# Kernel tuning notes

Measured on AMD Instinct MI355X. Metric: run time of the kernel, lower is better.

Reference implementation:

```python
import jax, jax.numpy as jnp
import numpy as np

E = 1024
H = 16
DH = E // H
FF = 4 * E
EPS = 1e-5


def _layer_norm(x, g, b):
    mu = jnp.mean(x, axis=-1, keepdims=True)
    var = jnp.var(x, axis=-1, keepdims=True)
    return (x - mu) * jax.lax.rsqrt(var + EPS) * g + b


def setup_inputs() -> dict:
    key = jax.random.key(0)
    ks = jax.random.split(key, 12)
    B, S = 2, 2048
    s_e = 1.0 / np.sqrt(E)
    s_f = 1.0 / np.sqrt(FF)
    return {
        "hidden_states": jax.random.normal(ks[0], (B, S, E), jnp.float32),
        "attention_mask": jnp.zeros((B, S), jnp.float32),
        "position_bias": jax.random.normal(ks[1], (H, S, S), jnp.float32) * 0.1,
        "Wq": jax.random.normal(ks[2], (E, E), jnp.float32) * s_e,
        "bq": jnp.zeros((E,), jnp.float32),
        "Wk": jax.random.normal(ks[3], (E, E), jnp.float32) * s_e,
        "bk": jnp.zeros((E,), jnp.float32),
        "Wv": jax.random.normal(ks[4], (E, E), jnp.float32) * s_e,
        "bv": jnp.zeros((E,), jnp.float32),
        "Wo": jax.random.normal(ks[5], (E, E), jnp.float32) * s_e,
        "bo": jnp.zeros((E,), jnp.float32),
        "ln1_g": jnp.ones((E,), jnp.float32),
        "ln1_b": jnp.zeros((E,), jnp.float32),
        "W1": jax.random.normal(ks[6], (E, FF), jnp.float32) * s_e,
        "b1": jnp.zeros((FF,), jnp.float32),
        "W2": jax.random.normal(ks[7], (FF, E), jnp.float32) * s_f,
        "b2": jnp.zeros((E,), jnp.float32),
        "ln2_g": jnp.ones((E,), jnp.float32),
        "ln2_b": jnp.zeros((E,), jnp.float32),
    }


def reference(hidden_states, attention_mask, position_bias, Wq, bq, Wk, bk, Wv, bv,
              Wo, bo, ln1_g, ln1_b, W1, b1, W2, b2, ln2_g, ln2_b):
    B, S, _ = hidden_states.shape
    x = hidden_states
    # QKV projections, split heads: [B, S, H, DH]
    q = (x @ Wq + bq).reshape(B, S, H, DH)
    k = (x @ Wk + bk).reshape(B, S, H, DH)
    v = (x @ Wv + bv).reshape(B, S, H, DH)
    # scores: [B, H, S, S]
    scores = jnp.einsum("bshd,bthd->bhst", q, k) / np.sqrt(DH).astype(np.float32)
    scores = scores + position_bias[None] + attention_mask[:, None, None, :]
    probs = jax.nn.softmax(scores, axis=-1)  # dropout is identity in eval
    ctx = jnp.einsum("bhst,bthd->bshd", probs, v).reshape(B, S, E)
    attn_out = ctx @ Wo + bo
    h = _layer_norm(x + attn_out, ln1_g, ln1_b)
    ffn = jax.nn.gelu(h @ W1 + b1, approximate=False) @ W2 + b2
    return _layer_norm(h + ffn, ln2_g, ln2_b)
```

## Files before the change

### kernel.cpp

```cpp
#include <hip/hip_runtime.h>
#include <stdint.h>

#define EDIM   1024
#define NHEAD  16
#define DHEAD  64
#define FFDIM  4096
#define SEQLEN 2048
#define NBATCH 2
#define MROWS  (NBATCH * SEQLEN)
#define NT     (SEQLEN / 64)

typedef __attribute__((ext_vector_type(8))) short bf16x8;
typedef __attribute__((ext_vector_type(4))) float f32x4;

static __device__ __forceinline__ unsigned short f2bf(float f) {
    union { float f; uint32_t u; } v; v.f = f;
    return (unsigned short)((v.u + 0x7fffu + ((v.u >> 16) & 1u)) >> 16);
}

static __device__ __forceinline__ void gload16(const void* g, void* s) {
    __builtin_amdgcn_global_load_lds(
        (const __attribute__((address_space(1))) unsigned int*)g,
        (__attribute__((address_space(3))) unsigned int*)s,
        16, 0, 0);
}

static __device__ __forceinline__ float gelu_f(float x) {
    float z = 0.7978845608028654f * (x + 0.044715f * x * x * x);
    float e = __expf(-2.0f * fabsf(z));
    float th = (1.0f - e) / (1.0f + e);
    th = (z >= 0.0f) ? th : -th;
    return 0.5f * x * (1.0f + th);
}

__global__ void k_cast_bf16(const float* __restrict__ in, unsigned short* __restrict__ out, int n4) {
    int i = blockIdx.x * blockDim.x + threadIdx.x;
    if (i < n4) {
        float4 v = ((const float4*)in)[i];
        ushort4 o;
        o.x = f2bf(v.x); o.y = f2bf(v.y); o.z = f2bf(v.z); o.w = f2bf(v.w);
        ((ushort4*)out)[i] = o;
    }
}

__global__ void k_transpose_cast(const float* __restrict__ in, unsigned short* __restrict__ out,
                                 int R, int C) {
    __shared__ float tile[32][33];
    int c0 = blockIdx.x * 32, r0 = blockIdx.y * 32;
    int tx = threadIdx.x, ty = threadIdx.y;
    #pragma unroll
    for (int i = 0; i < 32; i += 8)
        tile[ty + i][tx] = in[(size_t)(r0 + ty + i) * C + c0 + tx];
    __syncthreads();
    #pragma unroll
    for (int i = 0; i < 32; i += 8)
        out[(size_t)(c0 + ty + i) * R + r0 + tx] = f2bf(tile[tx][ty + i]);
}

__global__ void k_transpose_cast4(const float* __restrict__ s0, const float* __restrict__ s1,
                                  const float* __restrict__ s2, const float* __restrict__ s3,
                                  unsigned short* __restrict__ d0, unsigned short* __restrict__ d1,
                                  unsigned short* __restrict__ d2, unsigned short* __restrict__ d3) {
    __shared__ float tile[32][33];
    const int z = blockIdx.z;
    const float* in = (z == 0) ? s0 : (z == 1) ? s1 : (z == 2) ? s2 : s3;
    unsigned short* out = (z == 0) ? d0 : (z == 1) ? d1 : (z == 2) ? d2 : d3;
    int c0 = blockIdx.x * 32, r0 = blockIdx.y * 32;
    int tx = threadIdx.x, ty = threadIdx.y;
    #pragma unroll
    for (int i = 0; i < 32; i += 8)
        tile[ty + i][tx] = in[(size_t)(r0 + ty + i) * EDIM + c0 + tx];
    __syncthreads();
    #pragma unroll
    for (int i = 0; i < 32; i += 8)
        out[(size_t)(c0 + ty + i) * EDIM + r0 + tx] = f2bf(tile[tx][ty + i]);
}

__global__ void k_transpose_v(const unsigned short* __restrict__ V, int vstride,
                              unsigned short* __restrict__ Vt) {
    __shared__ unsigned short tile[32][33];
    const int bh = blockIdx.z, b = bh >> 4, h = bh & 15;
    const int s0 = blockIdx.x * 32, d0 = blockIdx.y * 32;
    const int tx = threadIdx.x, ty = threadIdx.y;
    #pragma unroll
    for (int i = 0; i < 32; i += 8)
        tile[ty + i][tx] = V[(size_t)(b * SEQLEN + s0 + ty + i) * vstride + h * DHEAD + d0 + tx];
    __syncthreads();
    #pragma unroll
    for (int i = 0; i < 32; i += 8)
        Vt[((size_t)(b * NHEAD + h) * DHEAD + d0 + ty + i) * SEQLEN + s0 + tx] = tile[tx][ty + i];
}

__global__ void k_concat_bias(const float* __restrict__ bq, const float* __restrict__ bk,
                              const float* __restrict__ bv, float* __restrict__ out) {
    int i = blockIdx.x * 256 + threadIdx.x;
    const float* src = (i < 1024) ? bq : (i < 2048) ? bk : bv;
    out[i] = src[i & 1023];
}

template <int TBM, int TBN, int EPI, int SPLITK>
__global__ __launch_bounds__(256, 3) void k_gemm(
    const unsigned short* __restrict__ A,
    const unsigned short* __restrict__ Bt,
    const float* __restrict__ bias,
    void* __restrict__ Cout, int M, int N, int K)
{
    constexpr int MR = TBM / 32, NR = TBN / 32;
    __shared__ __attribute__((aligned(16))) unsigned short Asm[TBM * 64];
    __shared__ __attribute__((aligned(16))) unsigned short Bsm[TBN * 64];

    const int nbx = gridDim.x;
    const int flat = blockIdx.y * nbx + blockIdx.x;
    const int cpx = (nbx * gridDim.y) >> 3;
    const int swz = (flat & 7) * cpx + (flat >> 3);
    const int bx = swz % nbx, by = swz / nbx;
    const int kz = (SPLITK > 1) ? blockIdx.z : 0;
    const int Ksub = K / SPLITK;

    const int row0 = by * TBM, col0 = bx * TBN;
    const int t = threadIdx.x;
    const int lane = t & 63, w = t >> 6;
    const int wm = w >> 1, wn = w & 1;
    const int l15 = lane & 15, l4 = lane >> 4;
    const int sr = lane >> 3, sc = (lane & 7) * 8;

    f32x4 acc[MR][NR];
    #pragma unroll
    for (int m = 0; m < MR; ++m)
        #pragma unroll
        for (int n = 0; n < NR; ++n) acc[m][n] = (f32x4){0.f, 0.f, 0.f, 0.f};

    for (int k0 = kz * Ksub; k0 < (kz + 1) * Ksub; k0 += 64) {
        #pragma unroll
        for (int i = 0; i < TBM / 32; ++i) {
            const int r = w * (TBM / 4) + i * 8;
            gload16(A + (size_t)(row0 + r + sr) * K + k0 + sc, &Asm[r * 64]);
        }
        #pragma unroll
        for (int i = 0; i < TBN / 32; ++i) {
            const int r = w * (TBN / 4) + i * 8;
            gload16(Bt + (size_t)(col0 + r + sr) * K + k0 + sc, &Bsm[r * 64]);
        }
        __syncthreads();
        #pragma unroll
        for (int kk = 0; kk < 64; kk += 32) {
            bf16x8 af[MR], bf[NR];
            #pragma unroll
            for (int m = 0; m < MR; ++m)
                af[m] = *(const bf16x8*)&Asm[(wm * (TBM / 2) + m * 16 + l15) * 64 + kk + l4 * 8];
            #pragma unroll
            for (int n = 0; n < NR; ++n)
                bf[n] = *(const bf16x8*)&Bsm[(wn * (TBN / 2) + n * 16 + l15) * 64 + kk + l4 * 8];
            #pragma unroll
            for (int m = 0; m < MR; ++m)
                #pragma unroll
                for (int n = 0; n < NR; ++n)
                    acc[m][n] = __builtin_amdgcn_mfma_f32_16x16x32_bf16(af[m], bf[n], acc[m][n], 0, 0, 0);
        }
        __syncthreads();
    }

    #pragma unroll
    for (int m = 0; m < MR; ++m) {
        int rb = row0 + wm * (TBM / 2) + m * 16 + l4 * 4;
        #pragma unroll
        for (int n = 0; n < NR; ++n) {
            int c = col0 + wn * (TBN / 2) + n * 16 + l15;
            float bv = (SPLITK == 1 || kz == 0) ? bias[c] : 0.0f;
            #pragma unroll
            for (int i = 0; i < 4; ++i) {
                float v = acc[m][n][i] + bv;
                if (EPI == 1) v = gelu_f(v);
                if (EPI == 2) {
                    float* outp = (float*)Cout + (size_t)kz * M * N;
                    outp[(size_t)(rb + i) * N + c] = v;
                } else {
                    ((unsigned short*)Cout)[(size_t)(rb + i) * N + c] = f2bf(v);
                }
            }
        }
    }
}

__global__ __launch_bounds__(512, 2) void k_attn(
    const unsigned short* __restrict__ QKV,
    const unsigned short* __restrict__ Vt,
    const float* __restrict__ pbias,
    const float* __restrict__ mask,
    unsigned short* __restrict__ Ctx)
{
    __shared__ __attribute__((aligned(16))) unsigned short Ksm[2][2][64 * 64];
    __shared__ __attribute__((aligned(16))) unsigned short Vsm[2][2][64 * 64];
    __shared__ __attribute__((aligned(16))) unsigned short Psm[8][16 * 32];

    const int flat = blockIdx.x;
    const int swz = (flat & 7) * 64 + (flat >> 3);
    const int qt = swz & 31;
    const int h  = swz >> 5;

    const int t = threadIdx.x;
    const int lane = t & 63, w = t >> 6;
    const int wb = w & 1;
    const int wq = (w >> 1) * 16;
    const int l15 = lane & 15, l4 = lane >> 4;
    const int qrow = qt * 64 + wq;

    const float* pbrow = pbias + ((size_t)h * SEQLEN + qrow + l4 * 4) * SEQLEN;
    const float* mrow  = mask + wb * SEQLEN;

    bf16x8 qf0, qf1;
    {
        const unsigned short* qp = QKV + (size_t)(wb * SEQLEN + qrow + l15) * (3 * EDIM) + h * DHEAD + l4 * 8;
        bf16x8 r0 = *(const bf16x8*)qp;
        bf16x8 r1 = *(const bf16x8*)(qp + 32);
        #pragma unroll
        for (int e = 0; e < 8; ++e) {
            union { uint32_t u; float f; } c0, c1;
            c0.u = (uint32_t)(unsigned short)r0[e] << 16;
            c1.u = (uint32_t)(unsigned short)r1[e] << 16;
            r0[e] = (short)f2bf(c0.f * 0.125f);
            r1[e] = (short)f2bf(c1.f * 0.125f);
        }
        qf0 = r0; qf1 = r1;
    }

    f32x4 oacc[4];
    #pragma unroll
    for (int nd = 0; nd < 4; ++nd) oacc[nd] = (f32x4){0.f, 0.f, 0.f, 0.f};
    float m_run[4] = {-1e30f, -1e30f, -1e30f, -1e30f};
    float l_run[4] = {0.f, 0.f, 0.f, 0.f};

    const int srow = lane >> 3;
    const int schk = lane & 7;
    const int r7 = l15 & 7;

    auto stage = [&](int buf, int kt) {
        const int kbase = kt * 64;
        #pragma unroll
        for (int j = 0; j < 4; ++j) {
            const int q  = w * 4 + j;
            const int kv = q >> 4;
            const int bb = (q >> 3) & 1;
            const int g  = q & 7;
            const int row = g * 8 + srow;
            const int cg  = (schk ^ (row & 7)) * 8;
            if (kv == 0)
                gload16(QKV + (size_t)(bb * SEQLEN + kbase + row) * (3 * EDIM) + EDIM + h * DHEAD + cg,
                        &Ksm[buf][bb][g * 512]);
            else
                gload16(Vt + ((size_t)((bb * NHEAD + h) * DHEAD) + row) * SEQLEN + kbase + cg,
                        &Vsm[buf][bb][g * 512]);
        }
    };

    auto compute = [&](int buf, int kt) {
        const int kbase = kt * 64;
        float p[4][4];
        float tmax[4] = {-1e30f, -1e30f, -1e30f, -1e30f};
        #pragma unroll
        for (int n = 0; n < 4; ++n) {
            const int scol = kbase + n * 16 + l15;
            const float mk = mrow[scol];
            f32x4 z;
            #pragma unroll
            for (int i = 0; i < 4; ++i) z[i] = pbrow[(size_t)i * SEQLEN + scol] + mk;
            bf16x8 kb0 = *(const bf16x8*)&Ksm[buf][wb][(n * 16 + l15) * 64 + ((l4 ^ r7) << 3)];
            bf16x8 kb1 = *(const bf16x8*)&Ksm[buf][wb][(n * 16 + l15) * 64 + (((4 + l4) ^ r7) << 3)];
            z = __builtin_amdgcn_mfma_f32_16x16x32_bf16(qf0, kb0, z, 0, 0, 0);
            z = __builtin_amdgcn_mfma_f32_16x16x32_bf16(qf1, kb1, z, 0, 0, 0);
            #pragma unroll
            for (int i = 0; i < 4; ++i) {
                p[n][i] = z[i];
                tmax[i] = fmaxf(tmax[i], z[i]);
            }
        }
        #pragma unroll
        for (int i = 0; i < 4; ++i) {
            float mv = tmax[i];
            #pragma unroll
            for (int off = 1; off < 16; off <<= 1) mv = fmaxf(mv, __shfl_xor(mv, off, 64));
            float mnew = fmaxf(m_run[i], mv);
            float alpha = __expf(m_run[i] - mnew);
            m_run[i] = mnew;
            float sum = 0.f;
            #pragma unroll
            for (int n = 0; n < 4; ++n) { p[n][i] = __expf(p[n][i] - mnew); sum += p[n][i]; }
            #pragma unroll
            for (int off = 1; off < 16; off <<= 1) sum += __shfl_xor(sum, off, 64);
            l_run[i] = l_run[i] * alpha + sum;
            #pragma unroll
            for (int nd = 0; nd < 4; ++nd) oacc[nd][i] *= alpha;
        }
        #pragma unroll
        for (int hh = 0; hh < 2; ++hh) {
            #pragma unroll
            for (int n = 0; n < 2; ++n)
                #pragma unroll
                for (int i = 0; i < 4; ++i) {
                    const int row = l4 * 4 + i;
                    const int cl = n * 16 + l15;
                    Psm[w][row * 32 + (((cl >> 3) ^ (row & 3)) << 3) + (cl & 7)] =
                        f2bf(p[2 * hh + n][i]);
                }
            bf16x8 pa = *(const bf16x8*)&Psm[w][l15 * 32 + ((l4 ^ (l15 & 3)) << 3)];
            #pragma unroll
            for (int nd = 0; nd < 4; ++nd) {
                bf16x8 vf = *(const bf16x8*)&Vsm[buf][wb][(nd * 16 + l15) * 64 + (((hh * 4 + l4) ^ r7) << 3)];
                oacc[nd] = __builtin_amdgcn_mfma_f32_16x16x32_bf16(pa, vf, oacc[nd], 0, 0, 0);
            }
        }
    };

    stage(0, 0);
    __syncthreads();
    int buf = 0;
    for (int kt = 0; kt < NT; ++kt) {
        stage(buf ^ 1, (kt + 1) & (NT - 1));
        compute(buf, kt);
        __syncthreads();
        buf ^= 1;
    }

    #pragma unroll
    for (int nd = 0; nd < 4; ++nd)
        #pragma unroll
        for (int i = 0; i < 4; ++i) {
            float v = oacc[nd][i] / l_run[i];
            Ctx[(size_t)(wb * SEQLEN + qrow + l4 * 4 + i) * EDIM + h * DHEAD + nd * 16 + l15] = f2bf(v);
        }
}

template <int WRITE_BF>
__global__ __launch_bounds__(256) void k_ln(
    const float* __restrict__ X, const float* __restrict__ T, const float* __restrict__ T2,
    const float* __restrict__ gam, const float* __restrict__ bet,
    float* __restrict__ Of, unsigned short* __restrict__ Ob)
{
    const int r = blockIdx.x;
    const int t = threadIdx.x;
    const size_t base = (size_t)r * EDIM + t * 4;
    float4 xv = *(const float4*)(X + base);
    float4 tv = *(const float4*)(T + base);
    float4 t2 = *(const float4*)(T2 + base);
    float4 s = make_float4(xv.x + tv.x + t2.x, xv.y + tv.y + t2.y,
                           xv.z + tv.z + t2.z, xv.w + tv.w + t2.w);
    float sum = s.x + s.y + s.z + s.w;
    float sq  = s.x * s.x + s.y * s.y + s.z * s.z + s.w * s.w;
    #pragma unroll
    for (int off = 1; off < 64; off <<= 1) {
        sum += __shfl_xor(sum, off, 64);
        sq  += __shfl_xor(sq,  off, 64);
    }
    __shared__ float red[8];
    const int lane = t & 63, w = t >> 6;
    if (lane == 0) { red[w] = sum; red[4 + w] = sq; }
    __syncthreads();
    sum = red[0] + red[1] + red[2] + red[3];
    sq  = red[4] + red[5] + red[6] + red[7];
    const float mu = sum * (1.0f / EDIM);
    const float var = sq * (1.0f / EDIM) - mu * mu;
    const float rs = rsqrtf(var + 1e-5f);
    float4 gv = *(const float4*)(gam + t * 4);
    float4 bv = *(const float4*)(bet + t * 4);
    float4 o = make_float4((s.x - mu) * rs * gv.x + bv.x,
                           (s.y - mu) * rs * gv.y + bv.y,
                           (s.z - mu) * rs * gv.z + bv.z,
                           (s.w - mu) * rs * gv.w + bv.w);
    *(float4*)(Of + base) = o;
    if (WRITE_BF) {
        ushort4 ob;
        ob.x = f2bf(o.x); ob.y = f2bf(o.y); ob.z = f2bf(o.z); ob.w = f2bf(o.w);
        *(ushort4*)(Ob + base) = ob;
    }
}

extern "C" void kernel_launch(void* const* d_in, const int* in_sizes, int n_in,
                              void* d_out, int out_size, void* d_ws, size_t ws_size,
                              hipStream_t stream) {
    const float* x    = (const float*)d_in[0];
    const float* mask = (const float*)d_in[1];
    const float* pb   = (const float*)d_in[2];
    const float* Wq = (const float*)d_in[3];  const float* bq = (const float*)d_in[4];
    const float* Wk = (const float*)d_in[5];  const float* bk = (const float*)d_in[6];
    const float* Wv = (const float*)d_in[7];  const float* bv = (const float*)d_in[8];
    const float* Wo = (const float*)d_in[9];  const float* bo = (const float*)d_in[10];
    const float* g1 = (const float*)d_in[11]; const float* be1 = (const float*)d_in[12];
    const float* W1 = (const float*)d_in[13]; const float* b1 = (const float*)d_in[14];
    const float* W2 = (const float*)d_in[15]; const float* b2 = (const float*)d_in[16];
    const float* g2 = (const float*)d_in[17]; const float* be2 = (const float*)d_in[18];
    float* out = (float*)d_out;

    char* ws = (char*)d_ws;
    const size_t MB = 1024 * 1024;
    unsigned short* qkv  = (unsigned short*)(ws + 0);
    unsigned short* gbf  = (unsigned short*)(ws + 0);
    unsigned short* wqt  = (unsigned short*)(ws + 32 * MB);
    unsigned short* wkt  = (unsigned short*)(ws + 34 * MB);
    unsigned short* wvt  = (unsigned short*)(ws + 36 * MB);
    unsigned short* wot  = (unsigned short*)(ws + 38 * MB);
    unsigned short* w1t  = (unsigned short*)(ws + 40 * MB);
    unsigned short* w2t  = (unsigned short*)(ws + 48 * MB);
    float*          bcat = (float*)(ws + 56 * MB);
    unsigned short* ctxb = (unsigned short*)(ws + 56 * MB);
    unsigned short* xb   = (unsigned short*)(ws + 64 * MB);
    unsigned short* vt   = (unsigned short*)(ws + 64 * MB);
    float*          pt0  = (float*)(ws + 72 * MB);
    float*          pt1  = (float*)(ws + 88 * MB);
    float*          hf   = (float*)(ws + 104 * MB);
    unsigned short* hb   = (unsigned short*)(ws + 120 * MB);

    const dim3 b256(256);
    const dim3 tb(32, 8);

    k_cast_bf16<<<dim3(MROWS * EDIM / 4 / 256), b256, 0, stream>>>(x, xb, MROWS * EDIM / 4);
    k_transpose_cast4<<<dim3(EDIM / 32, EDIM / 32, 4), tb, 0, stream>>>(
        Wq, Wk, Wv, Wo, wqt, wkt, wvt, wot);
    k_transpose_cast<<<dim3(FFDIM / 32, EDIM / 32), tb, 0, stream>>>(W1, w1t, EDIM, FFDIM);
    k_transpose_cast<<<dim3(EDIM / 32, FFDIM / 32), tb, 0, stream>>>(W2, w2t, FFDIM, EDIM);
    k_concat_bias<<<dim3(12), b256, 0, stream>>>(bq, bk, bv, bcat);

    k_gemm<128, 128, 0, 1><<<dim3(3 * EDIM / 128, MROWS / 128), b256, 0, stream>>>(
        xb, wqt, bcat, qkv, MROWS, 3 * EDIM, EDIM);
    k_transpose_v<<<dim3(SEQLEN / 32, DHEAD / 32, NBATCH * NHEAD), tb, 0, stream>>>(
        qkv + 2 * EDIM, 3 * EDIM, vt);

    k_attn<<<dim3(512), dim3(512), 0, stream>>>(qkv, vt, pb, mask, ctxb);

    k_gemm<128, 128, 2, 2><<<dim3(EDIM / 128, MROWS / 128, 2), b256, 0, stream>>>(
        ctxb, wot, bo, pt0, MROWS, EDIM, EDIM);
    k_ln<1><<<dim3(MROWS), b256, 0, stream>>>(x, pt0, pt1, g1, be1, hf, hb);
    k_gemm<128, 128, 1, 1><<<dim3(FFDIM / 128, MROWS / 128), b256, 0, stream>>>(
        hb, w1t, b1, gbf, MROWS, FFDIM, EDIM);
    k_gemm<128, 128, 2, 2><<<dim3(EDIM / 128, MROWS / 128, 2), b256, 0, stream>>>(
        gbf, w2t, b2, pt0, MROWS, EDIM, FFDIM);
    k_ln<0><<<dim3(MROWS), b256, 0, stream>>>(hf, pt0, pt1, g2, be2, out, nullptr);
    (void)in_sizes; (void)n_in; (void)out_size; (void)ws_size;
}
```

Baseline: 353.0 us.

## Give each attention block one batch and 128 query rows to halve LDS

Each attention workgroup now handles a single batch with 128 query rows (8 waves x 16 rows), where before it covered both batches with 64 rows each sharing the position-bias tile. This halves the K/V LDS staging buffers and raises the launch-bounds occupancy hint from 2 to 3 blocks per CU. The cost is that the position_bias rows are no longer shared across batches within a block, so bias reuse now depends on cache hits between separate blocks, and the block-to-head mapping changes.

```diff
diff --git a/kernel.cpp b/kernel.cpp
--- a/kernel.cpp
+++ b/kernel.cpp
@@ -182,35 +182,35 @@
     }
 }
 
-__global__ __launch_bounds__(512, 2) void k_attn(
+__global__ __launch_bounds__(512, 3) void k_attn(
     const unsigned short* __restrict__ QKV,
     const unsigned short* __restrict__ Vt,
     const float* __restrict__ pbias,
     const float* __restrict__ mask,
     unsigned short* __restrict__ Ctx)
 {
-    __shared__ __attribute__((aligned(16))) unsigned short Ksm[2][2][64 * 64];
-    __shared__ __attribute__((aligned(16))) unsigned short Vsm[2][2][64 * 64];
+    __shared__ __attribute__((aligned(16))) unsigned short Ksm[2][64 * 64];
+    __shared__ __attribute__((aligned(16))) unsigned short Vsm[2][64 * 64];
     __shared__ __attribute__((aligned(16))) unsigned short Psm[8][16 * 32];
 
     const int flat = blockIdx.x;
     const int swz = (flat & 7) * 64 + (flat >> 3);
-    const int qt = swz & 31;
-    const int h  = swz >> 5;
+    const int h   = swz >> 5;
+    const int rem = swz & 31;
+    const int b   = rem & 1;
+    const int qt  = rem >> 1;
 
     const int t = threadIdx.x;
     const int lane = t & 63, w = t >> 6;
-    const int wb = w & 1;
-    const int wq = (w >> 1) * 16;
     const int l15 = lane & 15, l4 = lane >> 4;
-    const int qrow = qt * 64 + wq;
+    const int qrow = qt * 128 + w * 16;
 
     const float* pbrow = pbias + ((size_t)h * SEQLEN + qrow + l4 * 4) * SEQLEN;
-    const float* mrow  = mask + wb * SEQLEN;
+    const float* mrow  = mask + b * SEQLEN;
 
     bf16x8 qf0, qf1;
     {
-        const unsigned short* qp = QKV + (size_t)(wb * SEQLEN + qrow + l15) * (3 * EDIM) + h * DHEAD + l4 * 8;
+        const unsigned short* qp = QKV + (size_t)(b * SEQLEN + qrow + l15) * (3 * EDIM) + h * DHEAD + l4 * 8;
         bf16x8 r0 = *(const bf16x8*)qp;
         bf16x8 r1 = *(const bf16x8*)(qp + 32);
         #pragma unroll
@@ -237,19 +237,18 @@
     auto stage = [&](int buf, int kt) {
         const int kbase = kt * 64;
         #pragma unroll
-        for (int j = 0; j < 4; ++j) {
-            const int q  = w * 4 + j;
-            const int kv = q >> 4;
-            const int bb = (q >> 3) & 1;
+        for (int j = 0; j < 2; ++j) {
+            const int q  = w * 2 + j;
+            const int kv = q >> 3;
             const int g  = q & 7;
             const int row = g * 8 + srow;
             const int cg  = (schk ^ (row & 7)) * 8;
             if (kv == 0)
-                gload16(QKV + (size_t)(bb * SEQLEN + kbase + row) * (3 * EDIM) + EDIM + h * DHEAD + cg,
-                        &Ksm[buf][bb][g * 512]);
+                gload16(QKV + (size_t)(b * SEQLEN + kbase + row) * (3 * EDIM) + EDIM + h * DHEAD + cg,
+                        &Ksm[buf][g * 512]);
             else
-                gload16(Vt + ((size_t)((bb * NHEAD + h) * DHEAD) + row) * SEQLEN + kbase + cg,
-                        &Vsm[buf][bb][g * 512]);
+                gload16(Vt + ((size_t)((b * NHEAD + h) * DHEAD) + row) * SEQLEN + kbase + cg,
+                        &Vsm[buf][g * 512]);
         }
     };
 
@@ -264,8 +263,8 @@
             f32x4 z;
             #pragma unroll
             for (int i = 0; i < 4; ++i) z[i] = pbrow[(size_t)i * SEQLEN + scol] + mk;
-            bf16x8 kb0 = *(const bf16x8*)&Ksm[buf][wb][(n * 16 + l15) * 64 + ((l4 ^ r7) << 3)];
-            bf16x8 kb1 = *(const bf16x8*)&Ksm[buf][wb][(n * 16 + l15) * 64 + (((4 + l4) ^ r7) << 3)];
+            bf16x8 kb0 = *(const bf16x8*)&Ksm[buf][(n * 16 + l15) * 64 + ((l4 ^ r7) << 3)];
+            bf16x8 kb1 = *(const bf16x8*)&Ksm[buf][(n * 16 + l15) * 64 + (((4 + l4) ^ r7) << 3)];
             z = __builtin_amdgcn_mfma_f32_16x16x32_bf16(qf0, kb0, z, 0, 0, 0);
             z = __builtin_amdgcn_mfma_f32_16x16x32_bf16(qf1, kb1, z, 0, 0, 0);
             #pragma unroll
@@ -305,7 +304,7 @@
             bf16x8 pa = *(const bf16x8*)&Psm[w][l15 * 32 + ((l4 ^ (l15 & 3)) << 3)];
             #pragma unroll
             for (int nd = 0; nd < 4; ++nd) {
-                bf16x8 vf = *(const bf16x8*)&Vsm[buf][wb][(nd * 16 + l15) * 64 + (((hh * 4 + l4) ^ r7) << 3)];
+                bf16x8 vf = *(const bf16x8*)&Vsm[buf][(nd * 16 + l15) * 64 + (((hh * 4 + l4) ^ r7) << 3)];
                 oacc[nd] = __builtin_amdgcn_mfma_f32_16x16x32_bf16(pa, vf, oacc[nd], 0, 0, 0);
             }
         }
@@ -326,7 +325,7 @@
         #pragma unroll
         for (int i = 0; i < 4; ++i) {
             float v = oacc[nd][i] / l_run[i];
-            Ctx[(size_t)(wb * SEQLEN + qrow + l4 * 4 + i) * EDIM + h * DHEAD + nd * 16 + l15] = f2bf(v);
+            Ctx[(size_t)(b * SEQLEN + qrow + l4 * 4 + i) * EDIM + h * DHEAD + nd * 16 + l15] = f2bf(v);
         }
 }
 
```

New measurement: 351.2 us, median of 2. Within noise of the previous version (-0.5%).
